# Performance work log

Measured on AMD Instinct MI355X. Metric: run time of the kernel, lower is better.

## Reference

```python
import jax, jax.numpy as jnp
import numpy as np

B, N, C = 2, 2048, 1024
H = 16
HD = C // H
GH = C // 4  # spatial gate hidden dim


def setup_inputs() -> dict:
    key = jax.random.key(0)
    ks = jax.random.split(key, 10)
    s = 0.02
    return {
        "x": jax.random.normal(ks[0], (B, N, C), dtype=jnp.float32),
        "spatial_mask": jax.random.uniform(ks[1], (B, N), dtype=jnp.float32),
        # qkv Linear: weight [3C, C], bias [3C] (torch convention: y = x @ W.T + b)
        "qkv_w": jax.random.normal(ks[2], (3 * C, C), dtype=jnp.float32) * s,
        "qkv_b": jnp.zeros((3 * C,), dtype=jnp.float32),
        # output proj Linear: weight [C, C], bias [C]
        "proj_w": jax.random.normal(ks[3], (C, C), dtype=jnp.float32) * s,
        "proj_b": jnp.zeros((C,), dtype=jnp.float32),
        # spatial_gate: Linear(1, C//4) -> ReLU -> Linear(C//4, 1) -> Sigmoid
        "g1_w": jax.random.normal(ks[4], (GH, 1), dtype=jnp.float32) * 0.5,
        "g1_b": jnp.zeros((GH,), dtype=jnp.float32),
        "g2_w": jax.random.normal(ks[5], (1, GH), dtype=jnp.float32) * 0.1,
        "g2_b": jnp.zeros((1,), dtype=jnp.float32),
    }


def reference(x, spatial_mask, qkv_w, qkv_b, proj_w, proj_b, g1_w, g1_b, g2_w, g2_b):
    b, n, c = x.shape
    # QKV projection: [B, N, 3C] -> [3, B, H, N, HD]
    qkv = (x @ qkv_w.T + qkv_b).reshape(b, n, 3, H, HD).transpose(2, 0, 3, 1, 4)
    q, k, v = qkv[0], qkv[1], qkv[2]

    # scaled attention scores [B, H, N, N]
    attn = jnp.einsum("bhqd,bhkd->bhqk", q, k) * (HD ** -0.5)

    # spatial gate on the mask: scalar MLP applied per key position
    m = spatial_mask[..., None]                      # [B, N, 1]
    h = jax.nn.relu(m @ g1_w.T + g1_b)               # [B, N, GH]
    gate = jax.nn.sigmoid(h @ g2_w.T + g2_b)         # [B, N, 1]
    gate = gate[:, None, None, :, 0]                 # [B, 1, 1, N] broadcasts over heads & queries

    attn = jax.nn.softmax(attn * gate, axis=-1)

    out = jnp.einsum("bhqk,bhkd->bhqd", attn, v)     # [B, H, N, HD]
    out = out.transpose(0, 2, 1, 3).reshape(b, n, c) # [B, N, C]
    return out @ proj_w.T + proj_b
```

## Files before the change

### kernel.cpp

```cpp
#include <hip/hip_runtime.h>

#define H 16
#define NSEQ 2048
#define HD 64
#define CDIM 1024

typedef __attribute__((ext_vector_type(8))) short s8v;
typedef __attribute__((ext_vector_type(4))) float f4v;
typedef __attribute__((ext_vector_type(16))) float f16v;

#define GLL(g, l) __builtin_amdgcn_global_load_lds( \
    (const __attribute__((address_space(1))) void*)(g), \
    (__attribute__((address_space(3))) void*)(l), 16, 0, 0)

__device__ __forceinline__ short f2bf(float f) {
  union { float f; unsigned u; } x; x.f = f;
  unsigned r = (x.u + 0x7fffu + ((x.u >> 16) & 1u)) >> 16;
  return (short)r;
}
__device__ __forceinline__ short f2bf_fast(float f) {
  return (short)((__float_as_uint(f) + 0x8000u) >> 16);
}
__device__ __forceinline__ unsigned pk(float a, float b) {
  unsigned ua = __float_as_uint(a) + 0x8000u;
  unsigned ub = __float_as_uint(b) + 0x8000u;
  return __builtin_amdgcn_perm(ub, ua, 0x07060302);
}

__global__ __launch_bounds__(256) void cvt3_kernel(
    const float* __restrict__ a, const float* __restrict__ b, const float* __restrict__ c,
    short* __restrict__ oa, short* __restrict__ ob, short* __restrict__ oc) {
  int i = blockIdx.x * 256 + threadIdx.x;
  const float* src; short* dst; int j;
  if (i < 1048576)      { src = a; dst = oa; j = i; }
  else if (i < 1835008) { src = b; dst = ob; j = i - 1048576; }
  else                  { src = c; dst = oc; j = i - 1835008; }
  float4 f = ((const float4*)src)[j];
  short4 s;
  s.x = f2bf(f.x); s.y = f2bf(f.y); s.z = f2bf(f.z); s.w = f2bf(f.w);
  ((short4*)dst)[j] = s;
}

__global__ __launch_bounds__(256) void gate_kernel(const float* __restrict__ mask,
    const float* __restrict__ g1w, const float* __restrict__ g1b,
    const float* __restrict__ g2w, const float* __restrict__ g2b,
    float* __restrict__ gate) {
  int i = blockIdx.x * 256 + threadIdx.x;
  float m = mask[i];
  float acc = 0.f;
  for (int j = 0; j < 256; j++) {
    float h = m * g1w[j] + g1b[j];
    h = fmaxf(h, 0.f);
    acc += g2w[j] * h;
  }
  gate[i] = 1.f / (1.f + __expf(-(acc + g2b[0])));
}

__global__ __launch_bounds__(256) void gemm_qkv(const short* __restrict__ X,
    const short* __restrict__ W, const float* __restrict__ bias, const float* __restrict__ gate,
    short* __restrict__ qws, short* __restrict__ kws, short* __restrict__ vtws) {
  __shared__ __align__(16) short At[4096];
  __shared__ __align__(16) short Bt[4096];
  const int K = CDIM;
  int tid = threadIdx.x;
  int lane = tid & 63, w = tid >> 6;
  int quad = lane >> 4, l15 = lane & 15;
  int wm = w >> 1, wn = w & 1;
  long rowBase = (long)blockIdx.y * 128;
  long colBase = (long)blockIdx.x * 128;
  const f4v fz = {0.f, 0.f, 0.f, 0.f};
  f4v acc[4][4];
#pragma unroll
  for (int i = 0; i < 4; i++)
#pragma unroll
    for (int j = 0; j < 4; j++) acc[i][j] = fz;

  int j0 = tid, j1 = 256 + tid;
  int sr0 = j0 >> 2, sp0 = j0 & 3, sc0 = sp0 ^ ((sr0 >> 1) & 3);
  int sr1 = j1 >> 2, sp1 = j1 & 3, sc1 = sp1 ^ ((sr1 >> 1) & 3);
  const short* Xa = X + (rowBase + sr0) * K + sc0 * 8;
  const short* Xb = X + (rowBase + sr1) * K + sc1 * 8;
  const short* Wa = W + (colBase + sr0) * K + sc0 * 8;
  const short* Wb = W + (colBase + sr1) * K + sc1 * 8;

  for (int k0 = 0; k0 < K; k0 += 32) {
    __syncthreads();
    GLL(Xa + k0, &At[j0 * 8]);
    GLL(Xb + k0, &At[j1 * 8]);
    GLL(Wa + k0, &Bt[j0 * 8]);
    GLL(Wb + k0, &Bt[j1 * 8]);
    __syncthreads();
    s8v a[4], b[4];
#pragma unroll
    for (int mi = 0; mi < 4; mi++) {
      int row = wm * 64 + mi * 16 + l15;
      a[mi] = *(const s8v*)&At[row * 32 + ((quad ^ ((row >> 1) & 3)) * 8)];
    }
#pragma unroll
    for (int ni = 0; ni < 4; ni++) {
      int row = wn * 64 + ni * 16 + l15;
      b[ni] = *(const s8v*)&Bt[row * 32 + ((quad ^ ((row >> 1) & 3)) * 8)];
    }
#pragma unroll
    for (int mi = 0; mi < 4; mi++)
#pragma unroll
      for (int ni = 0; ni < 4; ni++)
        acc[mi][ni] = __builtin_amdgcn_mfma_f32_16x16x32_bf16(a[mi], b[ni], acc[mi][ni], 0, 0, 0);
  }
#pragma unroll
  for (int mi = 0; mi < 4; mi++) {
    int row = (int)rowBase + wm * 64 + mi * 16 + quad * 4;
    int bb = row >> 11, nn = row & 2047;
#pragma unroll
    for (int ni = 0; ni < 4; ni++) {
      int col = (int)colBase + wn * 64 + ni * 16 + l15;
      int which = col >> 10, cc = col & 1023;
      int hh = cc >> 6, dd = cc & 63;
      float bcol = bias[col];
      if (which == 2) {
        short4 pv;
        pv.x = f2bf(acc[mi][ni][0] + bcol);
        pv.y = f2bf(acc[mi][ni][1] + bcol);
        pv.z = f2bf(acc[mi][ni][2] + bcol);
        pv.w = f2bf(acc[mi][ni][3] + bcol);
        *(short4*)&vtws[((bb * H + hh) * HD + dd) * NSEQ + nn] = pv;
      } else {
#pragma unroll
        for (int r = 0; r < 4; r++) {
          int rw = row + r;
          int idx = ((bb * H + hh) * NSEQ + (rw & 2047)) * HD + dd;
          float v = acc[mi][ni][r] + bcol;
          if (which == 0) qws[idx] = f2bf(v * 0.125f);
          else kws[idx] = f2bf(v * (gate[rw] * 1.44269504f));
        }
      }
    }
  }
}

__global__ __launch_bounds__(256) void gemm_proj(const short* __restrict__ X,
    const short* __restrict__ W, const float* __restrict__ bias, float* __restrict__ out) {
  __shared__ __align__(16) short At[4096];
  __shared__ __align__(16) short Bt[4096];
  const int K = CDIM;
  int tid = threadIdx.x;
  int lane = tid & 63, w = tid >> 6;
  int quad = lane >> 4, l15 = lane & 15;
  int wm = w >> 1, wn = w & 1;
  long rowBase = (long)blockIdx.y * 128;
  long colBase = (long)blockIdx.x * 128;
  const f4v fz = {0.f, 0.f, 0.f, 0.f};
  f4v acc[4][4];
#pragma unroll
  for (int i = 0; i < 4; i++)
#pragma unroll
    for (int j = 0; j < 4; j++) acc[i][j] = fz;

  int j0 = tid, j1 = 256 + tid;
  int sr0 = j0 >> 2, sp0 = j0 & 3, sc0 = sp0 ^ ((sr0 >> 1) & 3);
  int sr1 = j1 >> 2, sp1 = j1 & 3, sc1 = sp1 ^ ((sr1 >> 1) & 3);
  const short* Xa = X + (rowBase + sr0) * K + sc0 * 8;
  const short* Xb = X + (rowBase + sr1) * K + sc1 * 8;
  const short* Wa = W + (colBase + sr0) * K + sc0 * 8;
  const short* Wb = W + (colBase + sr1) * K + sc1 * 8;

  for (int k0 = 0; k0 < K; k0 += 32) {
    __syncthreads();
    GLL(Xa + k0, &At[j0 * 8]);
    GLL(Xb + k0, &At[j1 * 8]);
    GLL(Wa + k0, &Bt[j0 * 8]);
    GLL(Wb + k0, &Bt[j1 * 8]);
    __syncthreads();
    s8v a[4], b[4];
#pragma unroll
    for (int mi = 0; mi < 4; mi++) {
      int row = wm * 64 + mi * 16 + l15;
      a[mi] = *(const s8v*)&At[row * 32 + ((quad ^ ((row >> 1) & 3)) * 8)];
    }
#pragma unroll
    for (int ni = 0; ni < 4; ni++) {
      int row = wn * 64 + ni * 16 + l15;
      b[ni] = *(const s8v*)&Bt[row * 32 + ((quad ^ ((row >> 1) & 3)) * 8)];
    }
#pragma unroll
    for (int mi = 0; mi < 4; mi++)
#pragma unroll
      for (int ni = 0; ni < 4; ni++)
        acc[mi][ni] = __builtin_amdgcn_mfma_f32_16x16x32_bf16(a[mi], b[ni], acc[mi][ni], 0, 0, 0);
  }
#pragma unroll
  for (int mi = 0; mi < 4; mi++) {
    int row = (int)rowBase + wm * 64 + mi * 16 + quad * 4;
#pragma unroll
    for (int ni = 0; ni < 4; ni++) {
      int col = (int)colBase + wn * 64 + ni * 16 + l15;
      float bcol = bias[col];
#pragma unroll
      for (int r = 0; r < 4; r++)
        out[(long)(row + r) * CDIM + col] = acc[mi][ni][r] + bcol;
    }
  }
}

__global__ __launch_bounds__(256, 2) void attn_kernel(const short* __restrict__ qws,
    const short* __restrict__ kws, const short* __restrict__ vtws,
    short* __restrict__ attn_out) {
  __shared__ __align__(16) char smem[36864];
  short* Kt = (short*)smem;
  short* Vt = (short*)(smem + 8192);
  short* Pt = (short*)(smem + 16384);
  float* oscr = (float*)smem;
  float* lscr = (float*)(smem + 33792);
  float* linv = (float*)(smem + 34816);

  int tid = threadIdx.x;
  int lane = tid & 63, w = tid >> 6;
  int l31 = lane & 31, hf = lane >> 5;
  int wq = w >> 1, wk = w & 1;
  int sw = l31 & 7;
  int bh = blockIdx.x >> 4, qt = blockIdx.x & 15;
  int b = bh >> 4, head = bh & 15;
  int qbase = qt * 128;

  s8v qf[2][4];
  {
    const short* qp = qws + ((long)bh * NSEQ + qbase + wq * 64 + l31) * HD + hf * 8;
#pragma unroll
    for (int rt = 0; rt < 2; rt++)
#pragma unroll
      for (int ds = 0; ds < 4; ds++)
        qf[rt][ds] = *(const s8v*)&qp[rt * 32 * HD + ds * 16];
  }

  const f16v fz16 = {0.f,0.f,0.f,0.f,0.f,0.f,0.f,0.f,0.f,0.f,0.f,0.f,0.f,0.f,0.f,0.f};
  f16v oacc[2][2];
#pragma unroll
  for (int rt = 0; rt < 2; rt++)
#pragma unroll
    for (int nt = 0; nt < 2; nt++) oacc[rt][nt] = fz16;
  float l_r[2] = {0.f, 0.f};

  int r8 = lane >> 3, c8 = lane & 7;
  int row0 = w * 16 + r8, row1 = w * 16 + 8 + r8;
  const short* kg0 = kws + ((long)bh * NSEQ + row0) * HD + (c8 ^ (row0 & 7)) * 8;
  const short* kg1 = kws + ((long)bh * NSEQ + row1) * HD + (c8 ^ (row1 & 7)) * 8;
  const short* vg0 = vtws + ((long)bh * HD + row0) * NSEQ + (c8 ^ (row0 & 7)) * 8;
  const short* vg1 = vtws + ((long)bh * HD + row1) * NSEQ + (c8 ^ (row1 & 7)) * 8;
  short* kl0 = Kt + (w * 16) * 64;
  short* kl1 = Kt + (w * 16 + 8) * 64;
  short* vl0 = Vt + (w * 16) * 64;
  short* vl1 = Vt + (w * 16 + 8) * 64;

  const short* myKrow = Kt + (wk * 32 + l31) * 64;
  short* myP0 = Pt + ((w * 2 + 0) * 32 + l31) * 40;
  short* myP1 = Pt + ((w * 2 + 1) * 32 + l31) * 40;

  for (int kb = 0; kb < NSEQ; kb += 64) {
    __syncthreads();
    GLL(kg0 + (long)kb * HD, kl0);
    GLL(kg1 + (long)kb * HD, kl1);
    GLL(vg0 + kb, vl0);
    GLL(vg1 + kb, vl1);
    __syncthreads();

#pragma unroll
    for (int rt = 0; rt < 2; rt++) {
      f16v s = fz16;
#pragma unroll
      for (int ds = 0; ds < 4; ds++) {
        s8v ak = *(const s8v*)&myKrow[((2 * ds + hf) ^ sw) * 8];
        s = __builtin_amdgcn_mfma_f32_32x32x16_bf16(ak, qf[rt][ds], s, 0, 0, 0);
      }
      float p[16];
#pragma unroll
      for (int i = 0; i < 16; i++) p[i] = __builtin_amdgcn_exp2f(s[i]);
      float ls = 0.f;
#pragma unroll
      for (int i = 0; i < 16; i++) ls += p[i];
      ls += __shfl_xor(ls, 32);
      l_r[rt] += ls;
      short* myP = rt ? myP1 : myP0;
#pragma unroll
      for (int q = 0; q < 4; q++) {
        uint2 wv;
        wv.x = pk(p[4 * q], p[4 * q + 1]);
        wv.y = pk(p[4 * q + 2], p[4 * q + 3]);
        *(uint2*)&myP[8 * q + 4 * hf] = wv;
      }
    }
#pragma unroll
    for (int rt = 0; rt < 2; rt++) {
      short* myP = rt ? myP1 : myP0;
#pragma unroll
      for (int ks = 0; ks < 2; ks++) {
        s8v ap = *(const s8v*)&myP[ks * 16 + hf * 8];
#pragma unroll
        for (int nt = 0; nt < 2; nt++) {
          s8v bv = *(const s8v*)&Vt[(nt * 32 + l31) * 64 + (((4 * wk + 2 * ks + hf) ^ sw) * 8)];
          oacc[rt][nt] = __builtin_amdgcn_mfma_f32_32x32x16_bf16(ap, bv, oacc[rt][nt], 0, 0, 0);
        }
      }
    }
  }

  __syncthreads();
  if (wk == 1) {
#pragma unroll
    for (int rt = 0; rt < 2; rt++) {
      lscr[128 + wq * 64 + rt * 32 + l31] = l_r[rt];
#pragma unroll
      for (int nt = 0; nt < 2; nt++)
#pragma unroll
        for (int q = 0; q < 4; q++) {
          f4v t = {oacc[rt][nt][4 * q], oacc[rt][nt][4 * q + 1],
                   oacc[rt][nt][4 * q + 2], oacc[rt][nt][4 * q + 3]};
          *(f4v*)&oscr[(nt * 32 + l31) * 132 + wq * 64 + rt * 32 + 8 * q + 4 * hf] = t;
        }
    }
  } else {
#pragma unroll
    for (int rt = 0; rt < 2; rt++) lscr[wq * 64 + rt * 32 + l31] = l_r[rt];
  }
  __syncthreads();
  if (wk == 0) {
#pragma unroll
    for (int rt = 0; rt < 2; rt++) {
      float lt = l_r[rt] + lscr[128 + wq * 64 + rt * 32 + l31];
      linv[wq * 64 + rt * 32 + l31] = __builtin_amdgcn_rcpf(lt);
    }
#pragma unroll
    for (int rt = 0; rt < 2; rt++)
#pragma unroll
      for (int nt = 0; nt < 2; nt++) {
        int c = head * HD + nt * 32 + l31;
#pragma unroll
        for (int q = 0; q < 4; q++) {
          int rowbase = wq * 64 + rt * 32 + 8 * q + 4 * hf;
          f4v part = *(const f4v*)&oscr[(nt * 32 + l31) * 132 + rowbase];
          f4v li = *(const f4v*)&linv[rowbase];
#pragma unroll
          for (int r = 0; r < 4; r++) {
            float val = (oacc[rt][nt][4 * q + r] + part[r]) * li[r];
            int n = qbase + rowbase + r;
            attn_out[((long)b * NSEQ + n) * CDIM + c] = f2bf_fast(val);
          }
        }
      }
  }
}

extern "C" void kernel_launch(void* const* d_in, const int* in_sizes, int n_in,
                              void* d_out, int out_size, void* d_ws, size_t ws_size,
                              hipStream_t stream) {
  const float* x     = (const float*)d_in[0];
  const float* mask  = (const float*)d_in[1];
  const float* qkvw  = (const float*)d_in[2];
  const float* qkvb  = (const float*)d_in[3];
  const float* projw = (const float*)d_in[4];
  const float* projb = (const float*)d_in[5];
  const float* g1w   = (const float*)d_in[6];
  const float* g1b   = (const float*)d_in[7];
  const float* g2w   = (const float*)d_in[8];
  const float* g2b   = (const float*)d_in[9];
  float* out = (float*)d_out;

  char* ws = (char*)d_ws;
  short* x_bf    = (short*)(ws);
  short* w_qkv   = (short*)(ws + 8388608);
  short* w_proj  = (short*)(ws + 14680064);
  short* q_ws    = (short*)(ws + 16777216);
  short* k_ws    = (short*)(ws + 25165824);
  short* vt_ws   = (short*)(ws + 33554432);
  short* attn_bf = (short*)(ws + 41943040);
  float* gate    = (float*)(ws + 50331648);

  cvt3_kernel<<<8192, 256, 0, stream>>>(x, qkvw, projw, x_bf, w_qkv, w_proj);
  gate_kernel<<<16, 256, 0, stream>>>(mask, g1w, g1b, g2w, g2b, gate);

  dim3 gq(24, 32);
  gemm_qkv<<<gq, 256, 0, stream>>>(x_bf, w_qkv, qkvb, gate, q_ws, k_ws, vt_ws);

  attn_kernel<<<512, 256, 0, stream>>>(q_ws, k_ws, vt_ws, attn_bf);

  dim3 gp(8, 32);
  gemm_proj<<<gp, 256, 0, stream>>>(attn_bf, w_proj, projb, out);
}
```

Measured before the change: 239.6 us.

## Shrink attention and proj tiles, fuse gate into convert kernel

Attention query tile drops from 128 to 64 rows per block, so the grid grows to 1024 blocks. Launch bounds rise to 4 blocks per CU, shared memory shrinks, and blockIdx ordering is remapped so heads are interleaved. The proj GEMM row tile is halved to 64 to get more blocks. The gate MLP is folded into the conversion kernel to save a launch, and gate loads in the QKV epilogue are vectorized. Smaller tiles raise occupancy and parallelism but cut K/V reuse per block, which doubles K/V loads from memory.

```diff
diff --git a/kernel.cpp b/kernel.cpp
--- a/kernel.cpp
+++ b/kernel.cpp
@@ -27,10 +27,25 @@
   return __builtin_amdgcn_perm(ub, ua, 0x07060302);
 }
 
-__global__ __launch_bounds__(256) void cvt3_kernel(
+__global__ __launch_bounds__(256) void cvt_gate_kernel(
     const float* __restrict__ a, const float* __restrict__ b, const float* __restrict__ c,
-    short* __restrict__ oa, short* __restrict__ ob, short* __restrict__ oc) {
+    const float* __restrict__ mask,
+    const float* __restrict__ g1w, const float* __restrict__ g1b,
+    const float* __restrict__ g2w, const float* __restrict__ g2b,
+    short* __restrict__ oa, short* __restrict__ ob, short* __restrict__ oc,
+    float* __restrict__ gate) {
   int i = blockIdx.x * 256 + threadIdx.x;
+  if (i >= 2097152) {
+    int j = i - 2097152;
+    float m = mask[j];
+    float acc = 0.f;
+    for (int k = 0; k < 256; k++) {
+      float h = fmaxf(m * g1w[k] + g1b[k], 0.f);
+      acc += g2w[k] * h;
+    }
+    gate[j] = 1.f / (1.f + __expf(-(acc + g2b[0])));
+    return;
+  }
   const float* src; short* dst; int j;
   if (i < 1048576)      { src = a; dst = oa; j = i; }
   else if (i < 1835008) { src = b; dst = ob; j = i - 1048576; }
@@ -39,21 +54,6 @@
   short4 s;
   s.x = f2bf(f.x); s.y = f2bf(f.y); s.z = f2bf(f.z); s.w = f2bf(f.w);
   ((short4*)dst)[j] = s;
-}
-
-__global__ __launch_bounds__(256) void gate_kernel(const float* __restrict__ mask,
-    const float* __restrict__ g1w, const float* __restrict__ g1b,
-    const float* __restrict__ g2w, const float* __restrict__ g2b,
-    float* __restrict__ gate) {
-  int i = blockIdx.x * 256 + threadIdx.x;
-  float m = mask[i];
-  float acc = 0.f;
-  for (int j = 0; j < 256; j++) {
-    float h = m * g1w[j] + g1b[j];
-    h = fmaxf(h, 0.f);
-    acc += g2w[j] * h;
-  }
-  gate[i] = 1.f / (1.f + __expf(-(acc + g2b[0])));
 }
 
 __global__ __launch_bounds__(256) void gemm_qkv(const short* __restrict__ X,
@@ -111,6 +111,10 @@
   for (int mi = 0; mi < 4; mi++) {
     int row = (int)rowBase + wm * 64 + mi * 16 + quad * 4;
     int bb = row >> 11, nn = row & 2047;
+    f4v g4 = *(const f4v*)&gate[row];
+    float gl[4];
+#pragma unroll
+    for (int r = 0; r < 4; r++) gl[r] = g4[r] * 1.44269504f;
 #pragma unroll
     for (int ni = 0; ni < 4; ni++) {
       int col = (int)colBase + wn * 64 + ni * 16 + l15;
@@ -127,11 +131,10 @@
       } else {
 #pragma unroll
         for (int r = 0; r < 4; r++) {
-          int rw = row + r;
-          int idx = ((bb * H + hh) * NSEQ + (rw & 2047)) * HD + dd;
+          int idx = ((bb * H + hh) * NSEQ + nn + r) * HD + dd;
           float v = acc[mi][ni][r] + bcol;
           if (which == 0) qws[idx] = f2bf(v * 0.125f);
-          else kws[idx] = f2bf(v * (gate[rw] * 1.44269504f));
+          else kws[idx] = f2bf(v * gl[r]);
         }
       }
     }
@@ -140,41 +143,40 @@
 
 __global__ __launch_bounds__(256) void gemm_proj(const short* __restrict__ X,
     const short* __restrict__ W, const float* __restrict__ bias, float* __restrict__ out) {
-  __shared__ __align__(16) short At[4096];
+  __shared__ __align__(16) short At[2048];
   __shared__ __align__(16) short Bt[4096];
   const int K = CDIM;
   int tid = threadIdx.x;
   int lane = tid & 63, w = tid >> 6;
   int quad = lane >> 4, l15 = lane & 15;
   int wm = w >> 1, wn = w & 1;
-  long rowBase = (long)blockIdx.y * 128;
+  long rowBase = (long)blockIdx.y * 64;
   long colBase = (long)blockIdx.x * 128;
   const f4v fz = {0.f, 0.f, 0.f, 0.f};
-  f4v acc[4][4];
-#pragma unroll
-  for (int i = 0; i < 4; i++)
+  f4v acc[2][4];
+#pragma unroll
+  for (int i = 0; i < 2; i++)
 #pragma unroll
     for (int j = 0; j < 4; j++) acc[i][j] = fz;
 
   int j0 = tid, j1 = 256 + tid;
+  int sra = j0 >> 2, spa = j0 & 3, sca = spa ^ ((sra >> 1) & 3);
   int sr0 = j0 >> 2, sp0 = j0 & 3, sc0 = sp0 ^ ((sr0 >> 1) & 3);
   int sr1 = j1 >> 2, sp1 = j1 & 3, sc1 = sp1 ^ ((sr1 >> 1) & 3);
-  const short* Xa = X + (rowBase + sr0) * K + sc0 * 8;
-  const short* Xb = X + (rowBase + sr1) * K + sc1 * 8;
+  const short* Xa = X + (rowBase + sra) * K + sca * 8;
   const short* Wa = W + (colBase + sr0) * K + sc0 * 8;
   const short* Wb = W + (colBase + sr1) * K + sc1 * 8;
 
   for (int k0 = 0; k0 < K; k0 += 32) {
     __syncthreads();
     GLL(Xa + k0, &At[j0 * 8]);
-    GLL(Xb + k0, &At[j1 * 8]);
     GLL(Wa + k0, &Bt[j0 * 8]);
     GLL(Wb + k0, &Bt[j1 * 8]);
     __syncthreads();
-    s8v a[4], b[4];
-#pragma unroll
-    for (int mi = 0; mi < 4; mi++) {
-      int row = wm * 64 + mi * 16 + l15;
+    s8v a[2], b[4];
+#pragma unroll
+    for (int mi = 0; mi < 2; mi++) {
+      int row = wm * 32 + mi * 16 + l15;
       a[mi] = *(const s8v*)&At[row * 32 + ((quad ^ ((row >> 1) & 3)) * 8)];
     }
 #pragma unroll
@@ -183,14 +185,14 @@
       b[ni] = *(const s8v*)&Bt[row * 32 + ((quad ^ ((row >> 1) & 3)) * 8)];
     }
 #pragma unroll
-    for (int mi = 0; mi < 4; mi++)
+    for (int mi = 0; mi < 2; mi++)
 #pragma unroll
       for (int ni = 0; ni < 4; ni++)
         acc[mi][ni] = __builtin_amdgcn_mfma_f32_16x16x32_bf16(a[mi], b[ni], acc[mi][ni], 0, 0, 0);
   }
 #pragma unroll
-  for (int mi = 0; mi < 4; mi++) {
-    int row = (int)rowBase + wm * 64 + mi * 16 + quad * 4;
+  for (int mi = 0; mi < 2; mi++) {
+    int row = (int)rowBase + wm * 32 + mi * 16 + quad * 4;
 #pragma unroll
     for (int ni = 0; ni < 4; ni++) {
       int col = (int)colBase + wn * 64 + ni * 16 + l15;
@@ -202,46 +204,39 @@
   }
 }
 
-__global__ __launch_bounds__(256, 2) void attn_kernel(const short* __restrict__ qws,
+__global__ __launch_bounds__(256, 4) void attn_kernel(const short* __restrict__ qws,
     const short* __restrict__ kws, const short* __restrict__ vtws,
     short* __restrict__ attn_out) {
-  __shared__ __align__(16) char smem[36864];
+  __shared__ __align__(16) char smem[26624];
   short* Kt = (short*)smem;
   short* Vt = (short*)(smem + 8192);
   short* Pt = (short*)(smem + 16384);
   float* oscr = (float*)smem;
-  float* lscr = (float*)(smem + 33792);
-  float* linv = (float*)(smem + 34816);
+  float* lscr = (float*)(smem + 17408);
+  float* linv = (float*)(smem + 17664);
 
   int tid = threadIdx.x;
   int lane = tid & 63, w = tid >> 6;
   int l31 = lane & 31, hf = lane >> 5;
   int wq = w >> 1, wk = w & 1;
   int sw = l31 & 7;
-  int bh = blockIdx.x >> 4, qt = blockIdx.x & 15;
+  int bh = blockIdx.x & 31, qt = blockIdx.x >> 5;
   int b = bh >> 4, head = bh & 15;
-  int qbase = qt * 128;
-
-  s8v qf[2][4];
+  int qbase = qt * 64;
+
+  s8v qf[4];
   {
-    const short* qp = qws + ((long)bh * NSEQ + qbase + wq * 64 + l31) * HD + hf * 8;
-#pragma unroll
-    for (int rt = 0; rt < 2; rt++)
-#pragma unroll
-      for (int ds = 0; ds < 4; ds++)
-        qf[rt][ds] = *(const s8v*)&qp[rt * 32 * HD + ds * 16];
+    const short* qp = qws + ((long)bh * NSEQ + qbase + wq * 32 + l31) * HD + hf * 8;
+#pragma unroll
+    for (int ds = 0; ds < 4; ds++) qf[ds] = *(const s8v*)&qp[ds * 16];
   }
 
   const f16v fz16 = {0.f,0.f,0.f,0.f,0.f,0.f,0.f,0.f,0.f,0.f,0.f,0.f,0.f,0.f,0.f,0.f};
-  f16v oacc[2][2];
-#pragma unroll
-  for (int rt = 0; rt < 2; rt++)
-#pragma unroll
-    for (int nt = 0; nt < 2; nt++) oacc[rt][nt] = fz16;
-  float l_r[2] = {0.f, 0.f};
+  f16v oacc[2] = {fz16, fz16};
+  float l_r = 0.f;
 
   int r8 = lane >> 3, c8 = lane & 7;
-  int row0 = w * 16 + r8, row1 = w * 16 + 8 + r8;
+  int row0 = w * 16 + r8, row1 = row0 + 8;
   const short* kg0 = kws + ((long)bh * NSEQ + row0) * HD + (c8 ^ (row0 & 7)) * 8;
   const short* kg1 = kws + ((long)bh * NSEQ + row1) * HD + (c8 ^ (row1 & 7)) * 8;
   const short* vg0 = vtws + ((long)bh * HD + row0) * NSEQ + (c8 ^ (row0 & 7)) * 8;
@@ -252,8 +247,7 @@
   short* vl1 = Vt + (w * 16 + 8) * 64;
 
   const short* myKrow = Kt + (wk * 32 + l31) * 64;
-  short* myP0 = Pt + ((w * 2 + 0) * 32 + l31) * 40;
-  short* myP1 = Pt + ((w * 2 + 1) * 32 + l31) * 40;
+  short* myP = Pt + (w * 32 + l31) * 40;
 
   for (int kb = 0; kb < NSEQ; kb += 64) {
     __syncthreads();
@@ -263,89 +257,70 @@
     GLL(vg1 + kb, vl1);
     __syncthreads();
 
-#pragma unroll
-    for (int rt = 0; rt < 2; rt++) {
-      f16v s = fz16;
-#pragma unroll
-      for (int ds = 0; ds < 4; ds++) {
-        s8v ak = *(const s8v*)&myKrow[((2 * ds + hf) ^ sw) * 8];
-        s = __builtin_amdgcn_mfma_f32_32x32x16_bf16(ak, qf[rt][ds], s, 0, 0, 0);
+    f16v s = fz16;
+#pragma unroll
+    for (int ds = 0; ds < 4; ds++) {
+      s8v ak = *(const s8v*)&myKrow[((2 * ds + hf) ^ sw) * 8];
+      s = __builtin_amdgcn_mfma_f32_32x32x16_bf16(ak, qf[ds], s, 0, 0, 0);
+    }
+    float p[16];
+#pragma unroll
+    for (int i = 0; i < 16; i++) p[i] = __builtin_amdgcn_exp2f(s[i]);
+    float ls = 0.f;
+#pragma unroll
+    for (int i = 0; i < 16; i++) ls += p[i];
+    ls += __shfl_xor(ls, 32);
+    l_r += ls;
+#pragma unroll
+    for (int q = 0; q < 4; q++) {
+      uint2 wv;
+      wv.x = pk(p[4 * q], p[4 * q + 1]);
+      wv.y = pk(p[4 * q + 2], p[4 * q + 3]);
+      *(uint2*)&myP[8 * q + 4 * hf] = wv;
+    }
+#pragma unroll
+    for (int ks = 0; ks < 2; ks++) {
+      s8v ap = *(const s8v*)&myP[ks * 16 + hf * 8];
+#pragma unroll
+      for (int nt = 0; nt < 2; nt++) {
+        s8v bv = *(const s8v*)&Vt[(nt * 32 + l31) * 64 + (((4 * wk + 2 * ks + hf) ^ sw) * 8)];
+        oacc[nt] = __builtin_amdgcn_mfma_f32_32x32x16_bf16(ap, bv, oacc[nt], 0, 0, 0);
       }
-      float p[16];
-#pragma unroll
-      for (int i = 0; i < 16; i++) p[i] = __builtin_amdgcn_exp2f(s[i]);
-      float ls = 0.f;
-#pragma unroll
-      for (int i = 0; i < 16; i++) ls += p[i];
-      ls += __shfl_xor(ls, 32);
-      l_r[rt] += ls;
-      short* myP = rt ? myP1 : myP0;
+    }
+  }
+
+  __syncthreads();
+  if (wk == 1) {
+    lscr[wq * 32 + l31] = l_r;
+#pragma unroll
+    for (int nt = 0; nt < 2; nt++)
 #pragma unroll
       for (int q = 0; q < 4; q++) {
-        uint2 wv;
-        wv.x = pk(p[4 * q], p[4 * q + 1]);
-        wv.y = pk(p[4 * q + 2], p[4 * q + 3]);
-        *(uint2*)&myP[8 * q + 4 * hf] = wv;
+        f4v t = {oacc[nt][4 * q], oacc[nt][4 * q + 1],
+                 oacc[nt][4 * q + 2], oacc[nt][4 * q + 3]};
+        *(f4v*)&oscr[(nt * 32 + l31) * 68 + wq * 32 + 8 * q + 4 * hf] = t;
       }
-    }
-#pragma unroll
-    for (int rt = 0; rt < 2; rt++) {
-      short* myP = rt ? myP1 : myP0;
-#pragma unroll
-      for (int ks = 0; ks < 2; ks++) {
-        s8v ap = *(const s8v*)&myP[ks * 16 + hf * 8];
-#pragma unroll
-        for (int nt = 0; nt < 2; nt++) {
-          s8v bv = *(const s8v*)&Vt[(nt * 32 + l31) * 64 + (((4 * wk + 2 * ks + hf) ^ sw) * 8)];
-          oacc[rt][nt] = __builtin_amdgcn_mfma_f32_32x32x16_bf16(ap, bv, oacc[rt][nt], 0, 0, 0);
+  }
+  __syncthreads();
+  if (wk == 0) {
+    float lt = l_r + lscr[wq * 32 + l31];
+    linv[wq * 32 + l31] = __builtin_amdgcn_rcpf(lt);
+#pragma unroll
+    for (int nt = 0; nt < 2; nt++) {
+      int c = head * HD + nt * 32 + l31;
+#pragma unroll
+      for (int q = 0; q < 4; q++) {
+        int rowbase = wq * 32 + 8 * q + 4 * hf;
+        f4v part = *(const f4v*)&oscr[(nt * 32 + l31) * 68 + rowbase];
+        f4v li = *(const f4v*)&linv[rowbase];
+#pragma unroll
+        for (int r = 0; r < 4; r++) {
+          float val = (oacc[nt][4 * q + r] + part[r]) * li[r];
+          int n = qbase + rowbase + r;
+          attn_out[((long)b * NSEQ + n) * CDIM + c] = f2bf_fast(val);
         }
       }
     }
-  }
-
-  __syncthreads();
-  if (wk == 1) {
-#pragma unroll
-    for (int rt = 0; rt < 2; rt++) {
-      lscr[128 + wq * 64 + rt * 32 + l31] = l_r[rt];
-#pragma unroll
-      for (int nt = 0; nt < 2; nt++)
-#pragma unroll
-        for (int q = 0; q < 4; q++) {
-          f4v t = {oacc[rt][nt][4 * q], oacc[rt][nt][4 * q + 1],
-                   oacc[rt][nt][4 * q + 2], oacc[rt][nt][4 * q + 3]};
-          *(f4v*)&oscr[(nt * 32 + l31) * 132 + wq * 64 + rt * 32 + 8 * q + 4 * hf] = t;
-        }
-    }
-  } else {
-#pragma unroll
-    for (int rt = 0; rt < 2; rt++) lscr[wq * 64 + rt * 32 + l31] = l_r[rt];
-  }
-  __syncthreads();
-  if (wk == 0) {
-#pragma unroll
-    for (int rt = 0; rt < 2; rt++) {
-      float lt = l_r[rt] + lscr[128 + wq * 64 + rt * 32 + l31];
-      linv[wq * 64 + rt * 32 + l31] = __builtin_amdgcn_rcpf(lt);
-    }
-#pragma unroll
-    for (int rt = 0; rt < 2; rt++)
-#pragma unroll
-      for (int nt = 0; nt < 2; nt++) {
-        int c = head * HD + nt * 32 + l31;
-#pragma unroll
-        for (int q = 0; q < 4; q++) {
-          int rowbase = wq * 64 + rt * 32 + 8 * q + 4 * hf;
-          f4v part = *(const f4v*)&oscr[(nt * 32 + l31) * 132 + rowbase];
-          f4v li = *(const f4v*)&linv[rowbase];
-#pragma unroll
-          for (int r = 0; r < 4; r++) {
-            float val = (oacc[rt][nt][4 * q + r] + part[r]) * li[r];
-            int n = qbase + rowbase + r;
-            attn_out[((long)b * NSEQ + n) * CDIM + c] = f2bf_fast(val);
-          }
-        }
-      }
   }
 }
 
@@ -374,14 +349,14 @@
   short* attn_bf = (short*)(ws + 41943040);
   float* gate    = (float*)(ws + 50331648);
 
-  cvt3_kernel<<<8192, 256, 0, stream>>>(x, qkvw, projw, x_bf, w_qkv, w_proj);
-  gate_kernel<<<16, 256, 0, stream>>>(mask, g1w, g1b, g2w, g2b, gate);
+  cvt_gate_kernel<<<8208, 256, 0, stream>>>(x, qkvw, projw, mask, g1w, g1b, g2w, g2b,
+                                            x_bf, w_qkv, w_proj, gate);
 
   dim3 gq(24, 32);
   gemm_qkv<<<gq, 256, 0, stream>>>(x_bf, w_qkv, qkvb, gate, q_ws, k_ws, vt_ws);
 
-  attn_kernel<<<512, 256, 0, stream>>>(q_ws, k_ws, vt_ws, attn_bf);
-
-  dim3 gp(8, 32);
+  attn_kernel<<<1024, 256, 0, stream>>>(q_ws, k_ws, vt_ws, attn_bf);
+
+  dim3 gp(8, 64);
   gemm_proj<<<gp, 256, 0, stream>>>(attn_bf, w_proj, projb, out);
 }
```

Result: faster. 219.3 us (-8.5%).
